# Kernel tuning notes

Measured on AMD Instinct MI355X. Metric: run time of the kernel, lower is better.

## Reference

```python
import jax, jax.numpy as jnp
import numpy as np

NHEAD = 8
NEG_INF = -1e9
LN_EPS = 1e-5


def setup_inputs() -> dict:
    key = jax.random.key(0)
    ks = jax.random.split(key, 8)
    B, Q, N, C = 2, 256, 16384, 256
    return {
        "queries": jax.random.normal(ks[0], (B, Q, C), jnp.float32),
        "vid_features": jax.random.normal(ks[1], (B, C, N), jnp.float32),
        "vid_mask": jax.random.uniform(ks[2], (B, Q, N), jnp.float32),
        "pos_embed": jax.random.normal(ks[3], (B, C, N), jnp.float32),
        "query_embed": jax.random.normal(ks[4], (B, Q, C), jnp.float32),
        "in_proj_w": jax.random.normal(ks[5], (3 * C, C), jnp.float32) * 0.02,
        "in_proj_b": jnp.zeros((3 * C,), jnp.float32),
        "out_proj_w": jax.random.normal(ks[6], (C, C), jnp.float32) * 0.02,
        "out_proj_b": jnp.zeros((C,), jnp.float32),
        "ln_gamma": jnp.ones((C,), jnp.float32),
        "ln_beta": jnp.zeros((C,), jnp.float32),
    }


def reference(queries, vid_features, vid_mask, pos_embed, query_embed,
              in_proj_w, in_proj_b, out_proj_w, out_proj_b, ln_gamma, ln_beta):
    B, Q, C = queries.shape
    H = NHEAD
    d = C // H

    vf = jnp.transpose(vid_features, (0, 2, 1))   # B N C
    pe = jnp.transpose(pos_embed, (0, 2, 1))      # B N C

    q_in = queries + query_embed                  # with_pos_embed on queries
    k_in = vf + pe                                # with_pos_embed on keys
    v_in = vf

    wq, wk, wv = jnp.split(in_proj_w, 3, axis=0)
    bq, bk, bv = jnp.split(in_proj_b, 3)

    q = (q_in @ wq.T + bq).reshape(B, Q, H, d)
    k = (k_in @ wk.T + bk).reshape(B, -1, H, d)
    v = (v_in @ wv.T + bv).reshape(B, -1, H, d)

    scale = 1.0 / jnp.sqrt(jnp.asarray(d, q.dtype))
    logits = jnp.einsum('bqhd,bnhd->bhqn', q, k) * scale  # B H Q N

    # Hard masking: block keys where mask prob < 0.5; if a query row is
    # fully blocked, fall back to unmasked attention (avoid NaN softmax).
    blocked = vid_mask < 0.5                                 # B Q N
    all_blocked = jnp.all(blocked, axis=-1, keepdims=True)   # B Q 1
    blocked = blocked & jnp.logical_not(all_blocked)
    logits = jnp.where(blocked[:, None, :, :], NEG_INF, logits)

    attn = jax.nn.softmax(logits, axis=-1)
    ctx = jnp.einsum('bhqn,bnhd->bqhd', attn, v).reshape(B, Q, C)
    tgt2 = ctx @ out_proj_w.T + out_proj_b

    # residual + LayerNorm (dropout p=0.0 -> identity)
    x = queries + tgt2
    mu = jnp.mean(x, axis=-1, keepdims=True)
    var = jnp.mean(jnp.square(x - mu), axis=-1, keepdims=True)
    return (x - mu) / jnp.sqrt(var + LN_EPS) * ln_gamma + ln_beta
```

## Files before the change

### kernel.cpp

```cpp
#include <hip/hip_runtime.h>
#include <stdint.h>

#define B_ 2
#define Q_ 256
#define N_ 16384
#define C_ 256
#define H_ 8
#define D_ 32
#define NC_ 32
#define SCALE 0.17677669529663687f

typedef __bf16 bf16x8 __attribute__((ext_vector_type(8)));
typedef float f32x4 __attribute__((ext_vector_type(4)));

__device__ __forceinline__ uint16_t bfbits(float f) {
  union { __bf16 h; uint16_t u; } c; c.h = (__bf16)f; return c.u;
}
__device__ __forceinline__ float bf2f(uint16_t u) {
  union { uint32_t u; float f; } c; c.u = (uint32_t)u << 16;
  return c.f;
}
__device__ __forceinline__ uint32_t pk2(float a, float b) {
  union { struct { uint16_t lo, hi; } s; uint32_t u; } c;
  c.s.lo = bfbits(a); c.s.hi = bfbits(b);
  return c.u;
}
__device__ __forceinline__ void lgkm0_barrier() {
  __builtin_amdgcn_sched_barrier(0);
  asm volatile("s_waitcnt lgkmcnt(0)" ::: "memory");
  __builtin_amdgcn_sched_barrier(0);
  __builtin_amdgcn_s_barrier();
  __builtin_amdgcn_sched_barrier(0);
}

__global__ __launch_bounds__(256) void prep(const float* __restrict__ inw,
                                            const float* __restrict__ outw,
                                            const float* __restrict__ vm,
                                            uint16_t* __restrict__ wb,
                                            float* __restrict__ woT,
                                            uint32_t* __restrict__ mb) {
  __shared__ __align__(16) char sh[4352];
  const int bid = blockIdx.x;
  const int t = threadIdx.x;
  if (bid < 96) {
    const int i = (bid * 256 + t) * 8;
    const float4 a = *reinterpret_cast<const float4*>(inw + i);
    const float4 b = *reinterpret_cast<const float4*>(inw + i + 4);
    ushort4 lo = {bfbits(a.x), bfbits(a.y), bfbits(a.z), bfbits(a.w)};
    ushort4 hi = {bfbits(b.x), bfbits(b.y), bfbits(b.z), bfbits(b.w)};
    *reinterpret_cast<ushort4*>(wb + i) = lo;
    *reinterpret_cast<ushort4*>(wb + i + 4) = hi;
  } else if (bid < 160) {
    float(*s)[33] = reinterpret_cast<float(*)[33]>(sh);
    const int bb = bid - 96;
    const int bx = bb & 7, by = bb >> 3;
    const int r0 = by * 32, c0 = bx * 32;
    const int tr = t >> 5, tc = t & 31;
#pragma unroll
    for (int k = 0; k < 4; ++k)
      s[tr + 8 * k][tc] = outw[(size_t)(r0 + tr + 8 * k) * 256 + c0 + tc];
    __syncthreads();
#pragma unroll
    for (int k = 0; k < 4; ++k)
      woT[(size_t)(c0 + tr + 8 * k) * 256 + r0 + tc] = s[tc][tr + 8 * k];
  } else {
    uint8_t(*nib)[256] = reinterpret_cast<uint8_t(*)[256]>(sh);
    __shared__ int wcnt[4];
    __shared__ int tot;
    const int bq = bid - 160;
    const float* row = vm + (size_t)bq * N_;
    const int lane = t & 63;
    int cnt = 0;
#pragma unroll
    for (int i = 0; i < 16; ++i) {
      const float4 v = *reinterpret_cast<const float4*>(&row[i * 1024 + 4 * t]);
      const uint32_t nb = (v.x < 0.5f ? 1u : 0u) | (v.y < 0.5f ? 2u : 0u) |
                          (v.z < 0.5f ? 4u : 0u) | (v.w < 0.5f ? 8u : 0u);
      nib[i][t] = (uint8_t)nb;
      cnt += __popc(nb);
    }
    for (int o = 32; o > 0; o >>= 1) cnt += __shfl_down(cnt, o, 64);
    if (lane == 0) wcnt[t >> 6] = cnt;
    __syncthreads();
    if (t == 0) tot = wcnt[0] + wcnt[1] + wcnt[2] + wcnt[3];
    __syncthreads();
    const bool allb = (tot == N_);
    uint32_t* dst = mb + (size_t)bq * 512;
#pragma unroll
    for (int k = 0; k < 2; ++k) {
      const int w = k * 256 + t;
      const int i = w >> 5, tw = w & 31;
      const uint2 u = *reinterpret_cast<const uint2*>(&nib[i][8 * tw]);
      uint32_t y0 = u.x & 0x0F0F0F0Fu; y0 = y0 | (y0 >> 4);
      uint32_t y1 = u.y & 0x0F0F0F0Fu; y1 = y1 | (y1 >> 4);
      const uint32_t word = (y0 & 0xFFu) | (((y0 >> 16) & 0xFFu) << 8) |
                            ((y1 & 0xFFu) << 16) | (((y1 >> 16) & 0xFFu) << 24);
      dst[w] = allb ? 0u : word;
    }
  }
}

__global__ __launch_bounds__(512, 2) void kvqproj(const float* __restrict__ vf,
                                                  const float* __restrict__ pe,
                                                  const float* __restrict__ queries,
                                                  const float* __restrict__ qembed,
                                                  const uint16_t* __restrict__ wkv,
                                                  const float* __restrict__ bias,
                                                  uint16_t* __restrict__ Kh,
                                                  uint16_t* __restrict__ Vh,
                                                  uint16_t* __restrict__ Qb) {
  __shared__ __align__(16) uint16_t shpool[8][64][40];
  const int bid = blockIdx.x;
  const int t = threadIdx.x, wid = t >> 6, lane = t & 63;
  const int g = lane >> 4, c15 = lane & 15;

  if (bid >= 8) {
    const int kb = bid - 8;
    const int b = kb >> 8, nt = kb & 255;
    const int n0 = nt * 64;
    const int w = wid;

    const uint16_t* WsecK = wkv + (size_t)(256 + w * 32 + c15) * C_;
    const uint16_t* WsecV = wkv + (size_t)(512 + w * 32 + c15) * C_;

    f32x4 acck[8];
    f32x4 accv[8];
#pragma unroll
    for (int cf = 0; cf < 2; ++cf) {
      f32x4 ivk;
#pragma unroll
      for (int j = 0; j < 4; ++j) ivk[j] = bias[256 + w * 32 + cf * 16 + 4 * g + j];
      const float bv = bias[512 + w * 32 + cf * 16 + c15];
      const f32x4 ivv = {bv, bv, bv, bv};
#pragma unroll
      for (int nf = 0; nf < 4; ++nf) {
        acck[cf * 4 + nf] = ivk;
        accv[nf * 2 + cf] = ivv;
      }
    }

    const int cq = t >> 5, q2 = t & 31;
    const float* Xb = vf + ((size_t)b * C_ + 2 * cq) * N_ + n0 + 2 * q2;
    const float* Pb = pe + ((size_t)b * C_ + 2 * cq) * N_ + n0 + 2 * q2;
    const int cqs = cq ^ (((q2 >> 2) & 3) << 2);

    float2 xA0, xA1, pA0, pA1, xB0, xB1, pB0, pB1;
    bf16x8 Wk[2], Wv[2];

#define LOADW(s)                                                             \
    {                                                                        \
      _Pragma("unroll") for (int cf = 0; cf < 2; ++cf) {                     \
        Wk[cf] = *(const bf16x8*)(WsecK + (size_t)cf * 16 * C_ + (s) * 32 + g * 8); \
        Wv[cf] = *(const bf16x8*)(WsecV + (size_t)cf * 16 * C_ + (s) * 32 + g * 8); \
      }                                                                      \
    }
#define LOADA(X0, X1, P0, P1, s)                                             \
    {                                                                        \
      const float* x_ = Xb + (size_t)(s) * 32 * N_;                          \
      const float* p_ = Pb + (size_t)(s) * 32 * N_;                          \
      X0 = *(const float2*)x_;                                               \
      X1 = *(const float2*)(x_ + N_);                                        \
      P0 = *(const float2*)p_;                                               \
      P1 = *(const float2*)(p_ + N_);                                        \
    }
#define WRITEA(X0, X1, P0, P1, bufp)                                         \
    {                                                                        \
      *(uint32_t*)&shpool[bufp][2 * q2][2 * cqs]     = pk2(X0.x + P0.x, X1.x + P1.x); \
      *(uint32_t*)&shpool[bufp][2 * q2 + 1][2 * cqs] = pk2(X0.y + P0.y, X1.y + P1.y); \
      *(uint32_t*)&shpool[(bufp) + 1][2 * q2][2 * cqs]     = pk2(X0.x, X1.x); \
      *(uint32_t*)&shpool[(bufp) + 1][2 * q2 + 1][2 * cqs] = pk2(X0.y, X1.y); \
    }
#define COMPUTE(bufp)                                                        \
    {                                                                        \
      _Pragma("unroll") for (int nf = 0; nf < 4; ++nf) {                     \
        const int r_ = nf * 16 + c15;                                        \
        const int o_ = (g ^ ((r_ >> 3) & 3)) * 8;                            \
        const bf16x8 Fp = *(const bf16x8*)&shpool[bufp][r_][o_];             \
        const bf16x8 Fv = *(const bf16x8*)&shpool[(bufp) + 1][r_][o_];       \
        _Pragma("unroll") for (int cf = 0; cf < 2; ++cf) {                   \
          acck[cf * 4 + nf] = __builtin_amdgcn_mfma_f32_16x16x32_bf16(       \
              Wk[cf], Fp, acck[cf * 4 + nf], 0, 0, 0);                       \
          accv[nf * 2 + cf] = __builtin_amdgcn_mfma_f32_16x16x32_bf16(       \
              Fv, Wv[cf], accv[nf * 2 + cf], 0, 0, 0);                       \
        }                                                                    \
      }                                                                      \
    }

    LOADA(xA0, xA1, pA0, pA1, 0);
    LOADA(xB0, xB1, pB0, pB1, 1);
    LOADW(0); WRITEA(xA0, xA1, pA0, pA1, 0); LOADA(xA0, xA1, pA0, pA1, 2);
    lgkm0_barrier(); COMPUTE(0); __builtin_amdgcn_sched_barrier(0);
    LOADW(1); WRITEA(xB0, xB1, pB0, pB1, 2); LOADA(xB0, xB1, pB0, pB1, 3);
    lgkm0_barrier(); COMPUTE(2); __builtin_amdgcn_sched_barrier(0);
    LOADW(2); WRITEA(xA0, xA1, pA0, pA1, 0); LOADA(xA0, xA1, pA0, pA1, 4);
    lgkm0_barrier(); COMPUTE(0); __builtin_amdgcn_sched_barrier(0);
    LOADW(3); WRITEA(xB0, xB1, pB0, pB1, 2); LOADA(xB0, xB1, pB0, pB1, 5);
    lgkm0_barrier(); COMPUTE(2); __builtin_amdgcn_sched_barrier(0);
    LOADW(4); WRITEA(xA0, xA1, pA0, pA1, 0); LOADA(xA0, xA1, pA0, pA1, 6);
    lgkm0_barrier(); COMPUTE(0); __builtin_amdgcn_sched_barrier(0);
    LOADW(5); WRITEA(xB0, xB1, pB0, pB1, 2); LOADA(xB0, xB1, pB0, pB1, 7);
    lgkm0_barrier(); COMPUTE(2); __builtin_amdgcn_sched_barrier(0);
    LOADW(6); WRITEA(xA0, xA1, pA0, pA1, 0);
    lgkm0_barrier(); COMPUTE(0); __builtin_amdgcn_sched_barrier(0);
    LOADW(7); WRITEA(xB0, xB1, pB0, pB1, 2);
    lgkm0_barrier(); COMPUTE(2); __builtin_amdgcn_sched_barrier(0);

#undef LOADW
#undef LOADA
#undef WRITEA
#undef COMPUTE

    uint16_t* Kp = Kh + (size_t)(b * H_ + w) * N_ * D_;
#pragma unroll
    for (int cf = 0; cf < 2; ++cf)
#pragma unroll
      for (int nf = 0; nf < 4; ++nf) {
        const f32x4 a = acck[cf * 4 + nf];
        uint2 pkv;
        pkv.x = pk2(a[0], a[1]);
        pkv.y = pk2(a[2], a[3]);
        *(uint2*)&Kp[(size_t)(n0 + nf * 16 + c15) * D_ + cf * 16 + 4 * g] = pkv;
      }
    uint16_t* Vp = Vh + (size_t)(b * H_ + w) * D_ * N_;
#pragma unroll
    for (int nf = 0; nf < 4; ++nf)
#pragma unroll
      for (int cf = 0; cf < 2; ++cf) {
        const f32x4 a = accv[nf * 2 + cf];
        uint2 pkv;
        pkv.x = pk2(a[0], a[1]);
        pkv.y = pk2(a[2], a[3]);
        *(uint2*)&Vp[(size_t)(cf * 16 + c15) * N_ + n0 + nf * 16 + 4 * g] = pkv;
      }
  } else {
    const int qb = bid;
    const int q0g = qb * 64;
    const int b = q0g >> 8, q0 = q0g & 255;
    const int r = t >> 3, c0 = (t & 7) * 32, s = t & 7;
    const float* Qrow = queries + (size_t)(q0g + r) * C_ + c0;
    const float* Erow = qembed + (size_t)(q0g + r) * C_ + c0;
#pragma unroll
    for (int ph = 0; ph < 2; ++ph) {
      float4 a4[4], e4[4];
#pragma unroll
      for (int k = 0; k < 4; ++k) a4[k] = reinterpret_cast<const float4*>(Qrow + ph * 16)[k];
#pragma unroll
      for (int k = 0; k < 4; ++k) e4[k] = reinterpret_cast<const float4*>(Erow + ph * 16)[k];
      const float* af = reinterpret_cast<const float*>(a4);
      const float* ef = reinterpret_cast<const float*>(e4);
#pragma unroll
      for (int i = 0; i < 16; ++i) {
        const int cl = ph * 16 + i;
        const int col = cl ^ (8 * ((r >> 3) & 3));
        shpool[s][r][col] = bfbits(af[i] + ef[i]);
      }
      __builtin_amdgcn_sched_barrier(0);
    }
    lgkm0_barrier();

    const int w = wid;
    f32x4 acc[4][2];
#pragma unroll
    for (int nf = 0; nf < 2; ++nf) {
      const float bv = bias[w * 32 + nf * 16 + c15];
      const f32x4 iv = {bv, bv, bv, bv};
#pragma unroll
      for (int qf = 0; qf < 4; ++qf) acc[qf][nf] = iv;
    }
#pragma unroll
    for (int s8 = 0; s8 < 8; ++s8) {
      bf16x8 Bf[2];
#pragma unroll
      for (int nf = 0; nf < 2; ++nf)
        Bf[nf] = *reinterpret_cast<const bf16x8*>(
            wkv + (size_t)(w * 32 + nf * 16 + c15) * C_ + s8 * 32 + g * 8);
#pragma unroll
      for (int qf = 0; qf < 4; ++qf) {
        const int rr = qf * 16 + c15;
        const bf16x8 Af = *reinterpret_cast<const bf16x8*>(
            &shpool[s8][rr][8 * (g ^ ((rr >> 3) & 3))]);
#pragma unroll
        for (int nf = 0; nf < 2; ++nf)
          acc[qf][nf] = __builtin_amdgcn_mfma_f32_16x16x32_bf16(Af, Bf[nf], acc[qf][nf], 0, 0, 0);
      }
    }
#pragma unroll
    for (int qf = 0; qf < 4; ++qf)
#pragma unroll
      for (int nf = 0; nf < 2; ++nf)
#pragma unroll
        for (int j = 0; j < 4; ++j) {
          const int q = q0 + qf * 16 + 4 * g + j;
          const int dk = nf * 16 + c15;
          Qb[((size_t)(b * H_ + w) * Q_ + q) * D_ + dk] = bfbits(acc[qf][nf][j] * SCALE);
        }
  }
}

__global__ __launch_bounds__(512) void attn(const uint16_t* __restrict__ Qb,
                                            const uint16_t* __restrict__ Kh,
                                            const uint16_t* __restrict__ Vh,
                                            const uint32_t* __restrict__ mb,
                                            uint16_t* __restrict__ ctx_part,
                                            float* __restrict__ lsum_part) {
  const int bid = blockIdx.x;
  const int nc = bid & 31, h = (bid >> 5) & 7, b = bid >> 8;
  const int t = threadIdx.x, wid = t >> 6, lane = t & 63;
  const int g = lane >> 4, c15 = lane & 15;
  const int qw0 = wid * 32;
  const int nbase = nc * (N_ / NC_);
  constexpr int SS = (N_ / NC_) / 128;

  __shared__ __align__(16) uint16_t kst[2][128][40];
  __shared__ __align__(16) uint16_t vst[2][32][136];
  __shared__ __align__(16) uint16_t plds[8][32][40];

  const uint16_t* Qp = Qb + (size_t)(b * H_ + h) * Q_ * D_;
  bf16x8 qfr[2];
#pragma unroll
  for (int qf = 0; qf < 2; ++qf)
    qfr[qf] = *reinterpret_cast<const bf16x8*>(Qp + (size_t)(qw0 + qf * 16 + c15) * D_ + g * 8);

  f32x4 acc[2][2];
  const f32x4 zero4 = {0.f, 0.f, 0.f, 0.f};
#pragma unroll
  for (int qf = 0; qf < 2; ++qf)
#pragma unroll
    for (int dvf = 0; dvf < 2; ++dvf) acc[qf][dvf] = zero4;
  float lsum[2][4] = {};

  const uint32_t* mrow = mb + (size_t)b * Q_ * (N_ / 32);

  const int krow = t >> 2, kch = t & 3;
  const uint16_t* ksrc = Kh + ((size_t)(b * H_ + h) * N_ + nbase + krow) * 32 + kch * 8;
  const int vrow = t >> 4, vch = t & 15;
  const uint16_t* vsrc = Vh + ((size_t)(b * H_ + h) * 32 + vrow) * N_ + nbase + vch * 8;

  uint4 kreg = *(const uint4*)ksrc;
  uint4 vreg = *(const uint4*)vsrc;

  int cur = 0;
  for (int ss = 0; ss < SS; ++ss) {
    *(uint4*)&kst[cur][krow][kch * 8] = kreg;
    *(uint4*)&vst[cur][vrow][vch * 8] = vreg;
    if (ss < SS - 1) {
      kreg = *(const uint4*)(ksrc + (size_t)(ss + 1) * 128 * 32);
      vreg = *(const uint4*)(vsrc + (ss + 1) * 128);
    }
    lgkm0_barrier();

    const int nstart = nbase + ss * 128;
#pragma unroll
    for (int half = 0; half < 2; ++half) {
      uint32_t mw[2][4][2];
#pragma unroll
      for (int qf = 0; qf < 2; ++qf)
#pragma unroll
        for (int j = 0; j < 4; ++j) {
          const int q = qw0 + qf * 16 + 4 * g + j;
          const uint2 u = *reinterpret_cast<const uint2*>(
              &mrow[(size_t)q * (N_ / 32) + (nstart >> 5) + half * 2]);
          mw[qf][j][0] = u.x;
          mw[qf][j][1] = u.y;
        }
#pragma unroll
      for (int s2 = 0; s2 < 2; ++s2) {
        const int sub = half * 2 + s2;
        const int nl0 = sub * 32;
        bf16x8 kfr[2];
#pragma unroll
        for (int nf = 0; nf < 2; ++nf)
          kfr[nf] = *reinterpret_cast<const bf16x8*>(&kst[cur][nl0 + nf * 16 + c15][g * 8]);
        f32x4 s[2][2];
#pragma unroll
        for (int qf = 0; qf < 2; ++qf)
#pragma unroll
          for (int nf = 0; nf < 2; ++nf)
            s[qf][nf] = __builtin_amdgcn_mfma_f32_16x16x32_bf16(qfr[qf], kfr[nf], zero4, 0, 0, 0);

#pragma unroll
        for (int qf = 0; qf < 2; ++qf) {
#pragma unroll
          for (int j = 0; j < 4; ++j) {
            const uint32_t wmask = mw[qf][j][s2];
#pragma unroll
            for (int nf = 0; nf < 2; ++nf) {
              const int bit = nf * 16 + c15;
              const float p = ((wmask >> bit) & 1u) ? 0.0f : __expf(s[qf][nf][j]);
              lsum[qf][j] += p;
              plds[wid][qf * 16 + 4 * g + j][nf * 16 + c15] = bfbits(p);
            }
          }
        }
        __asm__ volatile("s_waitcnt lgkmcnt(0)" ::: "memory");
#pragma unroll
        for (int qf = 0; qf < 2; ++qf) {
          const bf16x8 pa = *reinterpret_cast<const bf16x8*>(&plds[wid][qf * 16 + c15][g * 8]);
#pragma unroll
          for (int dvf = 0; dvf < 2; ++dvf) {
            const bf16x8 vb =
                *reinterpret_cast<const bf16x8*>(&vst[cur][dvf * 16 + c15][nl0 + g * 8]);
            acc[qf][dvf] = __builtin_amdgcn_mfma_f32_16x16x32_bf16(pa, vb, acc[qf][dvf], 0, 0, 0);
          }
        }
      }
    }
    __builtin_amdgcn_sched_barrier(0);
    cur ^= 1;
  }

#pragma unroll
  for (int qf = 0; qf < 2; ++qf)
#pragma unroll
    for (int j = 0; j < 4; ++j) {
      float v = lsum[qf][j];
      v += __shfl_xor(v, 1, 64);
      v += __shfl_xor(v, 2, 64);
      v += __shfl_xor(v, 4, 64);
      v += __shfl_xor(v, 8, 64);
      lsum[qf][j] = v;
    }

  uint16_t* cp = ctx_part + ((size_t)(b * H_ + h) * NC_ + nc) * Q_ * D_;
#pragma unroll
  for (int qf = 0; qf < 2; ++qf)
#pragma unroll
    for (int dvf = 0; dvf < 2; ++dvf)
#pragma unroll
      for (int j = 0; j < 4; ++j) {
        const int q = qw0 + qf * 16 + 4 * g + j;
        cp[(size_t)q * D_ + dvf * 16 + c15] = bfbits(acc[qf][dvf][j]);
      }
  if (c15 == 0) {
    float* lp = lsum_part + ((size_t)(b * H_ + h) * NC_ + nc) * Q_;
#pragma unroll
    for (int qf = 0; qf < 2; ++qf)
#pragma unroll
      for (int j = 0; j < 4; ++j) lp[qw0 + qf * 16 + 4 * g + j] = lsum[qf][j];
  }
}

__global__ __launch_bounds__(256) void epilogue(const uint16_t* __restrict__ ctx_part,
                                                const float* __restrict__ lsum_part,
                                                const float* __restrict__ queries,
                                                const float* __restrict__ woT,
                                                const float* __restrict__ bo,
                                                const float* __restrict__ gamma,
                                                const float* __restrict__ beta,
                                                float* __restrict__ out) {
  const int bq = blockIdx.x;
  const int b = bq >> 8, q = bq & 255;
  const int t = threadIdx.x;
  const int h = t >> 5, dv = t & 31;
  float cs = 0.f, ls = 0.f;
#pragma unroll 8
  for (int k = 0; k < NC_; ++k) {
    cs += bf2f(ctx_part[(((size_t)(b * H_ + h) * NC_ + k) * Q_ + q) * D_ + dv]);
    ls += lsum_part[((size_t)(b * H_ + h) * NC_ + k) * Q_ + q];
  }
  __shared__ float ctxrow[C_];
  ctxrow[t] = cs / ls;
  __syncthreads();
  float acc = bo[t];
#pragma unroll 8
  for (int j = 0; j < C_; ++j) acc = fmaf(ctxrow[j], woT[(size_t)j * C_ + t], acc);
  const float x = queries[(size_t)bq * C_ + t] + acc;
  float s1 = x, s2 = x * x;
  for (int o = 32; o > 0; o >>= 1) {
    s1 += __shfl_down(s1, o, 64);
    s2 += __shfl_down(s2, o, 64);
  }
  __shared__ float r1[4], r2[4];
  if ((t & 63) == 0) { r1[t >> 6] = s1; r2[t >> 6] = s2; }
  __syncthreads();
  const float mu = (r1[0] + r1[1] + r1[2] + r1[3]) * (1.0f / C_);
  const float e2 = (r2[0] + r2[1] + r2[2] + r2[3]) * (1.0f / C_);
  const float var = e2 - mu * mu;
  out[(size_t)bq * C_ + t] = (x - mu) * rsqrtf(var + 1e-5f) * gamma[t] + beta[t];
}

extern "C" void kernel_launch(void* const* d_in, const int* in_sizes, int n_in,
                              void* d_out, int out_size, void* d_ws, size_t ws_size,
                              hipStream_t stream) {
  const float* queries    = (const float*)d_in[0];
  const float* vidfeat    = (const float*)d_in[1];
  const float* vidmask    = (const float*)d_in[2];
  const float* posembed   = (const float*)d_in[3];
  const float* queryembed = (const float*)d_in[4];
  const float* inw        = (const float*)d_in[5];
  const float* inb        = (const float*)d_in[6];
  const float* outw       = (const float*)d_in[7];
  const float* outb       = (const float*)d_in[8];
  const float* gamma      = (const float*)d_in[9];
  const float* beta       = (const float*)d_in[10];
  float* out = (float*)d_out;

  char* ws = (char*)d_ws;
  size_t off = 0;
  uint16_t* Qb   = (uint16_t*)(ws + off); off += (size_t)B_ * H_ * Q_ * D_ * 2;
  uint16_t* Kh   = (uint16_t*)(ws + off); off += (size_t)B_ * H_ * N_ * D_ * 2;
  uint16_t* Vh   = (uint16_t*)(ws + off); off += (size_t)B_ * H_ * D_ * N_ * 2;
  uint32_t* mb   = (uint32_t*)(ws + off); off += (size_t)B_ * Q_ * (N_ / 32) * 4;
  uint16_t* wkv  = (uint16_t*)(ws + off); off += (size_t)768 * C_ * 2;
  float* woT     = (float*)(ws + off);    off += (size_t)C_ * C_ * 4;
  uint16_t* ctxp = (uint16_t*)(ws + off); off += (size_t)B_ * H_ * NC_ * Q_ * D_ * 2;
  float* lsump   = (float*)(ws + off);    off += (size_t)B_ * H_ * NC_ * Q_ * 4;

  prep<<<dim3(672), dim3(256), 0, stream>>>(inw, outw, vidmask, wkv, woT, mb);
  kvqproj<<<dim3(520), dim3(512), 0, stream>>>(vidfeat, posembed, queries, queryembed,
                                               wkv, inb, Kh, Vh, Qb);
  attn<<<dim3(B_ * H_ * NC_), dim3(512), 0, stream>>>(Qb, Kh, Vh, mb, ctxp, lsump);
  epilogue<<<dim3(B_ * Q_), dim3(256), 0, stream>>>(ctxp, lsump, queries, woT, outb,
                                                    gamma, beta, out);
}
```

Measured before the change: 95.20 us.

## Fold prep kernel into projection kernel and use exp2 with log2e-scaled queries

```diff
diff --git a/kernel.cpp b/kernel.cpp
--- a/kernel.cpp
+++ b/kernel.cpp
@@ -8,7 +8,7 @@
 #define H_ 8
 #define D_ 32
 #define NC_ 32
-#define SCALE 0.17677669529663687f
+#define SCALEQ 0.2550542176432015f
 
 typedef __bf16 bf16x8 __attribute__((ext_vector_type(8)));
 typedef float f32x4 __attribute__((ext_vector_type(4)));
@@ -24,6 +24,12 @@
   union { struct { uint16_t lo, hi; } s; uint32_t u; } c;
   c.s.lo = bfbits(a); c.s.hi = bfbits(b);
   return c.u;
+}
+__device__ __forceinline__ bf16x8 pack8(const float4 a, const float4 b) {
+  union { uint32_t u[4]; bf16x8 v; } c;
+  c.u[0] = pk2(a.x, a.y); c.u[1] = pk2(a.z, a.w);
+  c.u[2] = pk2(b.x, b.y); c.u[3] = pk2(b.z, b.w);
+  return c.v;
 }
 __device__ __forceinline__ void lgkm0_barrier() {
   __builtin_amdgcn_sched_barrier(0);
@@ -33,95 +39,34 @@
   __builtin_amdgcn_sched_barrier(0);
 }
 
-__global__ __launch_bounds__(256) void prep(const float* __restrict__ inw,
-                                            const float* __restrict__ outw,
-                                            const float* __restrict__ vm,
-                                            uint16_t* __restrict__ wb,
-                                            float* __restrict__ woT,
-                                            uint32_t* __restrict__ mb) {
-  __shared__ __align__(16) char sh[4352];
-  const int bid = blockIdx.x;
-  const int t = threadIdx.x;
-  if (bid < 96) {
-    const int i = (bid * 256 + t) * 8;
-    const float4 a = *reinterpret_cast<const float4*>(inw + i);
-    const float4 b = *reinterpret_cast<const float4*>(inw + i + 4);
-    ushort4 lo = {bfbits(a.x), bfbits(a.y), bfbits(a.z), bfbits(a.w)};
-    ushort4 hi = {bfbits(b.x), bfbits(b.y), bfbits(b.z), bfbits(b.w)};
-    *reinterpret_cast<ushort4*>(wb + i) = lo;
-    *reinterpret_cast<ushort4*>(wb + i + 4) = hi;
-  } else if (bid < 160) {
-    float(*s)[33] = reinterpret_cast<float(*)[33]>(sh);
-    const int bb = bid - 96;
-    const int bx = bb & 7, by = bb >> 3;
-    const int r0 = by * 32, c0 = bx * 32;
-    const int tr = t >> 5, tc = t & 31;
-#pragma unroll
-    for (int k = 0; k < 4; ++k)
-      s[tr + 8 * k][tc] = outw[(size_t)(r0 + tr + 8 * k) * 256 + c0 + tc];
-    __syncthreads();
-#pragma unroll
-    for (int k = 0; k < 4; ++k)
-      woT[(size_t)(c0 + tr + 8 * k) * 256 + r0 + tc] = s[tc][tr + 8 * k];
-  } else {
-    uint8_t(*nib)[256] = reinterpret_cast<uint8_t(*)[256]>(sh);
-    __shared__ int wcnt[4];
-    __shared__ int tot;
-    const int bq = bid - 160;
-    const float* row = vm + (size_t)bq * N_;
-    const int lane = t & 63;
-    int cnt = 0;
-#pragma unroll
-    for (int i = 0; i < 16; ++i) {
-      const float4 v = *reinterpret_cast<const float4*>(&row[i * 1024 + 4 * t]);
-      const uint32_t nb = (v.x < 0.5f ? 1u : 0u) | (v.y < 0.5f ? 2u : 0u) |
-                          (v.z < 0.5f ? 4u : 0u) | (v.w < 0.5f ? 8u : 0u);
-      nib[i][t] = (uint8_t)nb;
-      cnt += __popc(nb);
-    }
-    for (int o = 32; o > 0; o >>= 1) cnt += __shfl_down(cnt, o, 64);
-    if (lane == 0) wcnt[t >> 6] = cnt;
-    __syncthreads();
-    if (t == 0) tot = wcnt[0] + wcnt[1] + wcnt[2] + wcnt[3];
-    __syncthreads();
-    const bool allb = (tot == N_);
-    uint32_t* dst = mb + (size_t)bq * 512;
-#pragma unroll
-    for (int k = 0; k < 2; ++k) {
-      const int w = k * 256 + t;
-      const int i = w >> 5, tw = w & 31;
-      const uint2 u = *reinterpret_cast<const uint2*>(&nib[i][8 * tw]);
-      uint32_t y0 = u.x & 0x0F0F0F0Fu; y0 = y0 | (y0 >> 4);
-      uint32_t y1 = u.y & 0x0F0F0F0Fu; y1 = y1 | (y1 >> 4);
-      const uint32_t word = (y0 & 0xFFu) | (((y0 >> 16) & 0xFFu) << 8) |
-                            ((y1 & 0xFFu) << 16) | (((y1 >> 16) & 0xFFu) << 24);
-      dst[w] = allb ? 0u : word;
-    }
-  }
-}
-
 __global__ __launch_bounds__(512, 2) void kvqproj(const float* __restrict__ vf,
                                                   const float* __restrict__ pe,
                                                   const float* __restrict__ queries,
                                                   const float* __restrict__ qembed,
-                                                  const uint16_t* __restrict__ wkv,
+                                                  const float* __restrict__ inw,
+                                                  const float* __restrict__ outw,
+                                                  const float* __restrict__ vm,
                                                   const float* __restrict__ bias,
                                                   uint16_t* __restrict__ Kh,
                                                   uint16_t* __restrict__ Vh,
-                                                  uint16_t* __restrict__ Qb) {
+                                                  uint16_t* __restrict__ Qb,
+                                                  float* __restrict__ woT,
+                                                  uint32_t* __restrict__ mb) {
   __shared__ __align__(16) uint16_t shpool[8][64][40];
+  __shared__ int wcnt[8];
+  __shared__ int tot;
   const int bid = blockIdx.x;
   const int t = threadIdx.x, wid = t >> 6, lane = t & 63;
   const int g = lane >> 4, c15 = lane & 15;
 
-  if (bid >= 8) {
-    const int kb = bid - 8;
+  if (bid >= 8 && bid < 1032 && ((bid - 8) & 1) == 0) {
+    const int kb = (bid - 8) >> 1;
     const int b = kb >> 8, nt = kb & 255;
     const int n0 = nt * 64;
     const int w = wid;
 
-    const uint16_t* WsecK = wkv + (size_t)(256 + w * 32 + c15) * C_;
-    const uint16_t* WsecV = wkv + (size_t)(512 + w * 32 + c15) * C_;
+    const float* WrK = inw + (size_t)(256 + w * 32 + c15) * C_;
+    const float* WrV = inw + (size_t)(512 + w * 32 + c15) * C_;
 
     f32x4 acck[8];
     f32x4 accv[8];
@@ -150,8 +95,10 @@
 #define LOADW(s)                                                             \
     {                                                                        \
       _Pragma("unroll") for (int cf = 0; cf < 2; ++cf) {                     \
-        Wk[cf] = *(const bf16x8*)(WsecK + (size_t)cf * 16 * C_ + (s) * 32 + g * 8); \
-        Wv[cf] = *(const bf16x8*)(WsecV + (size_t)cf * 16 * C_ + (s) * 32 + g * 8); \
+        const float* wk_ = WrK + (size_t)cf * 16 * C_ + (s) * 32 + g * 8;    \
+        const float* wv_ = WrV + (size_t)cf * 16 * C_ + (s) * 32 + g * 8;    \
+        Wk[cf] = pack8(*(const float4*)wk_, *(const float4*)(wk_ + 4));      \
+        Wv[cf] = pack8(*(const float4*)wv_, *(const float4*)(wv_ + 4));      \
       }                                                                      \
     }
 #define LOADA(X0, X1, P0, P1, s)                                             \
@@ -232,9 +179,53 @@
         pkv.y = pk2(a[2], a[3]);
         *(uint2*)&Vp[(size_t)(cf * 16 + c15) * N_ + n0 + nf * 16 + 4 * g] = pkv;
       }
+  } else if (bid >= 8 && bid < 1032) {
+    const int bq = (bid - 8) >> 1;
+    uint8_t(*nib)[512] = reinterpret_cast<uint8_t(*)[512]>(&shpool[0][0][0]);
+    const float* row = vm + (size_t)bq * N_;
+    int cnt = 0;
+#pragma unroll
+    for (int i = 0; i < 8; ++i) {
+      const float4 v = *reinterpret_cast<const float4*>(&row[i * 2048 + 4 * t]);
+      const uint32_t nb = (v.x < 0.5f ? 1u : 0u) | (v.y < 0.5f ? 2u : 0u) |
+                          (v.z < 0.5f ? 4u : 0u) | (v.w < 0.5f ? 8u : 0u);
+      nib[i][t] = (uint8_t)nb;
+      cnt += __popc(nb);
+    }
+    for (int o = 32; o > 0; o >>= 1) cnt += __shfl_down(cnt, o, 64);
+    if (lane == 0) wcnt[wid] = cnt;
+    __syncthreads();
+    if (t == 0) {
+      int s = 0;
+#pragma unroll
+      for (int k = 0; k < 8; ++k) s += wcnt[k];
+      tot = s;
+    }
+    __syncthreads();
+    const bool allb = (tot == N_);
+    const int w = t;
+    const uint2 u = *reinterpret_cast<const uint2*>(&nib[w >> 6][8 * (w & 63)]);
+    uint32_t y0 = u.x & 0x0F0F0F0Fu; y0 = y0 | (y0 >> 4);
+    uint32_t y1 = u.y & 0x0F0F0F0Fu; y1 = y1 | (y1 >> 4);
+    const uint32_t word = (y0 & 0xFFu) | (((y0 >> 16) & 0xFFu) << 8) |
+                          ((y1 & 0xFFu) << 16) | (((y1 >> 16) & 0xFFu) << 24);
+    mb[(size_t)bq * 512 + w] = allb ? 0u : word;
+  } else if (bid >= 1032) {
+    float(*s)[32][33] = reinterpret_cast<float(*)[32][33]>(&shpool[0][0][0]);
+    const int half = t >> 8, tt = t & 255;
+    const int bb = (bid - 1032) * 2 + half;
+    const int bx = bb & 7, by = bb >> 3;
+    const int r0 = by * 32, c0 = bx * 32;
+    const int tr = tt >> 5, tc = tt & 31;
+#pragma unroll
+    for (int k = 0; k < 4; ++k)
+      s[half][tr + 8 * k][tc] = outw[(size_t)(r0 + tr + 8 * k) * 256 + c0 + tc];
+    __syncthreads();
+#pragma unroll
+    for (int k = 0; k < 4; ++k)
+      woT[(size_t)(c0 + tr + 8 * k) * 256 + r0 + tc] = s[half][tc][tr + 8 * k];
   } else {
-    const int qb = bid;
-    const int q0g = qb * 64;
+    const int q0g = bid * 64;
     const int b = q0g >> 8, q0 = q0g & 255;
     const int r = t >> 3, c0 = (t & 7) * 32, s = t & 7;
     const float* Qrow = queries + (size_t)(q0g + r) * C_ + c0;
@@ -271,9 +262,10 @@
     for (int s8 = 0; s8 < 8; ++s8) {
       bf16x8 Bf[2];
 #pragma unroll
-      for (int nf = 0; nf < 2; ++nf)
-        Bf[nf] = *reinterpret_cast<const bf16x8*>(
-            wkv + (size_t)(w * 32 + nf * 16 + c15) * C_ + s8 * 32 + g * 8);
+      for (int nf = 0; nf < 2; ++nf) {
+        const float* wr = inw + (size_t)(w * 32 + nf * 16 + c15) * C_ + s8 * 32 + g * 8;
+        Bf[nf] = pack8(*(const float4*)wr, *(const float4*)(wr + 4));
+      }
 #pragma unroll
       for (int qf = 0; qf < 4; ++qf) {
         const int rr = qf * 16 + c15;
@@ -292,7 +284,7 @@
         for (int j = 0; j < 4; ++j) {
           const int q = q0 + qf * 16 + 4 * g + j;
           const int dk = nf * 16 + c15;
-          Qb[((size_t)(b * H_ + w) * Q_ + q) * D_ + dk] = bfbits(acc[qf][nf][j] * SCALE);
+          Qb[((size_t)(b * H_ + w) * Q_ + q) * D_ + dk] = bfbits(acc[qf][nf][j] * SCALEQ);
         }
   }
 }
@@ -386,7 +378,7 @@
 #pragma unroll
             for (int nf = 0; nf < 2; ++nf) {
               const int bit = nf * 16 + c15;
-              const float p = ((wmask >> bit) & 1u) ? 0.0f : __expf(s[qf][nf][j]);
+              const float p = ((wmask >> bit) & 1u) ? 0.0f : exp2f(s[qf][nf][j]);
               lsum[qf][j] += p;
               plds[wid][qf * 16 + 4 * g + j][nf * 16 + c15] = bfbits(p);
             }
@@ -501,14 +493,13 @@
   uint16_t* Kh   = (uint16_t*)(ws + off); off += (size_t)B_ * H_ * N_ * D_ * 2;
   uint16_t* Vh   = (uint16_t*)(ws + off); off += (size_t)B_ * H_ * D_ * N_ * 2;
   uint32_t* mb   = (uint32_t*)(ws + off); off += (size_t)B_ * Q_ * (N_ / 32) * 4;
-  uint16_t* wkv  = (uint16_t*)(ws + off); off += (size_t)768 * C_ * 2;
   float* woT     = (float*)(ws + off);    off += (size_t)C_ * C_ * 4;
   uint16_t* ctxp = (uint16_t*)(ws + off); off += (size_t)B_ * H_ * NC_ * Q_ * D_ * 2;
   float* lsump   = (float*)(ws + off);    off += (size_t)B_ * H_ * NC_ * Q_ * 4;
 
-  prep<<<dim3(672), dim3(256), 0, stream>>>(inw, outw, vidmask, wkv, woT, mb);
-  kvqproj<<<dim3(520), dim3(512), 0, stream>>>(vidfeat, posembed, queries, queryembed,
-                                               wkv, inb, Kh, Vh, Qb);
+  kvqproj<<<dim3(1064), dim3(512), 0, stream>>>(vidfeat, posembed, queries, queryembed,
+                                                inw, outw, vidmask, inb,
+                                                Kh, Vh, Qb, woT, mb);
   attn<<<dim3(B_ * H_ * NC_), dim3(512), 0, stream>>>(Qb, Kh, Vh, mb, ctxp, lsump);
   epilogue<<<dim3(B_ * Q_), dim3(256), 0, stream>>>(ctxp, lsump, queries, woT, outb,
                                                     gamma, beta, out);
```

Measured after the change: 159.3 us. 67.4% more time.
